# Kernel tuning notes

Measured on AMD Instinct MI355X. Metric: run time of the kernel, lower is better.

## Reference

```python
import jax, jax.numpy as jnp
import numpy as np

HEADS, DH, M, ITERS = 8, 64, 256, 6
DIM = 512


def layer_norm(x, g, b, eps=1e-5):
    mu = x.mean(-1, keepdims=True)
    var = x.var(-1, keepdims=True)
    return (x - mu) / jnp.sqrt(var + eps) * g + b


def moore_penrose_pinv(x, iters=ITERS):
    abs_x = jnp.abs(x)
    col = abs_x.sum(-1)
    row = abs_x.sum(-2)
    z = jnp.swapaxes(x, -1, -2) / (jnp.max(col) * jnp.max(row))
    I = jnp.eye(x.shape[-1], dtype=x.dtype)
    for _ in range(iters):
        xz = x @ z
        z = 0.25 * z @ (13.0 * I - xz @ (15.0 * I - xz @ (7.0 * I - xz)))
    return z


def nystrom_attn(x, w_qkv, w_out, b_out, res_w):
    b, n, _ = x.shape
    pad = (M - n % M) % M
    xp = jnp.pad(x, ((0, 0), (pad, 0), (0, 0)))  # left-pad seq as in lucidrains
    npad = n + pad
    l = npad // M  # == ceil(n / M)
    qkv = xp @ w_qkv
    q, k, v = jnp.split(qkv, 3, axis=-1)
    to_heads = lambda t: t.reshape(b, npad, HEADS, DH).transpose(0, 2, 1, 3)
    q, k, v = to_heads(q), to_heads(k), to_heads(v)
    q = q * (DH ** -0.5)
    # landmarks: mean over consecutive chunks of size l  ('(n l) d -> n d')
    ql = q.reshape(b, HEADS, M, l, DH).mean(3)
    kl = k.reshape(b, HEADS, M, l, DH).mean(3)
    a1 = jax.nn.softmax(jnp.einsum('bhid,bhjd->bhij', q, kl), -1)   # (b,h,npad,M)
    a2 = jax.nn.softmax(jnp.einsum('bhid,bhjd->bhij', ql, kl), -1)  # (b,h,M,M)
    a3 = jax.nn.softmax(jnp.einsum('bhid,bhjd->bhij', ql, k), -1)   # (b,h,M,npad)
    a2inv = moore_penrose_pinv(a2)
    out = a1 @ (a2inv @ (a3 @ v))  # (b,h,npad,DH)
    # residual depthwise conv along sequence, per head (kernel (33,1), groups=heads)
    res = jax.lax.conv_general_dilated(v, res_w, window_strides=(1, 1),
                                       padding=((16, 16), (0, 0)),
                                       dimension_numbers=('NCHW', 'OIHW', 'NCHW'),
                                       feature_group_count=HEADS)
    out = out + res
    out = out.transpose(0, 2, 1, 3).reshape(b, npad, HEADS * DH)
    out = out @ w_out + b_out
    return out[:, -n:]


def ppeg(x, w7, b7, w5, b5, w3, b3, Hh, Ww):
    B, n, C = x.shape
    cls_tok, feat = x[:, :1], x[:, 1:]
    cnn = feat.transpose(0, 2, 1).reshape(B, C, Hh, Ww)

    def dwconv(w, bb, p):
        y = jax.lax.conv_general_dilated(cnn, w, (1, 1), ((p, p), (p, p)),
                                         dimension_numbers=('NCHW', 'OIHW', 'NCHW'),
                                         feature_group_count=C)
        return y + bb[None, :, None, None]

    y = cnn + dwconv(w7, b7, 3) + dwconv(w5, b5, 2) + dwconv(w3, b3, 1)
    y = y.reshape(B, C, Hh * Ww).transpose(0, 2, 1)
    return jnp.concatenate([cls_tok, y], axis=1)


def setup_inputs() -> dict:
    key = jax.random.key(0)
    ks = iter(jax.random.split(key, 32))
    rn = lambda shape, s=0.02: jax.random.normal(next(ks), shape, dtype=jnp.float32) * s
    inp = {
        'data': jax.random.normal(next(ks), (1, 16000, 1024), dtype=jnp.float32),
        'fc1_w': rn((1024, 512)), 'fc1_b': jnp.zeros((512,), jnp.float32),
        'cls_token': rn((1, 1, 512), 1.0),
        'l1_norm_g': jnp.ones((512,), jnp.float32), 'l1_norm_b': jnp.zeros((512,), jnp.float32),
        'l1_qkv_w': rn((512, 1536)), 'l1_out_w': rn((512, 512)), 'l1_out_b': jnp.zeros((512,), jnp.float32),
        'l1_res_w': rn((8, 1, 33, 1)),
        'ppeg_w7': rn((512, 1, 7, 7)), 'ppeg_b7': jnp.zeros((512,), jnp.float32),
        'ppeg_w5': rn((512, 1, 5, 5)), 'ppeg_b5': jnp.zeros((512,), jnp.float32),
        'ppeg_w3': rn((512, 1, 3, 3)), 'ppeg_b3': jnp.zeros((512,), jnp.float32),
        'l2_norm_g': jnp.ones((512,), jnp.float32), 'l2_norm_b': jnp.zeros((512,), jnp.float32),
        'l2_qkv_w': rn((512, 1536)), 'l2_out_w': rn((512, 512)), 'l2_out_b': jnp.zeros((512,), jnp.float32),
        'l2_res_w': rn((8, 1, 33, 1)),
        'norm_g': jnp.ones((512,), jnp.float32), 'norm_b': jnp.zeros((512,), jnp.float32),
        'fc2_w': rn((512, 2)), 'fc2_b': jnp.zeros((2,), jnp.float32),
    }
    return inp


def reference(data, fc1_w, fc1_b, cls_token, l1_norm_g, l1_norm_b, l1_qkv_w, l1_out_w,
              l1_out_b, l1_res_w, ppeg_w7, ppeg_b7, ppeg_w5, ppeg_b5, ppeg_w3, ppeg_b3,
              l2_norm_g, l2_norm_b, l2_qkv_w, l2_out_w, l2_out_b, l2_res_w,
              norm_g, norm_b, fc2_w, fc2_b):
    h = jax.nn.relu(data @ fc1_w + fc1_b)  # (B, N, 512)
    N = h.shape[1]
    s = int(np.ceil(np.sqrt(N)))  # square grid side
    add = s * s - N
    h = jnp.concatenate([h, h[:, :add]], axis=1)  # repeat-pad to s*s
    B = h.shape[0]
    cls = jnp.broadcast_to(cls_token, (B, 1, h.shape[2]))
    h = jnp.concatenate([cls, h], axis=1)  # (B, s*s+1, 512)
    h = h + nystrom_attn(layer_norm(h, l1_norm_g, l1_norm_b), l1_qkv_w, l1_out_w, l1_out_b, l1_res_w)
    h = ppeg(h, ppeg_w7, ppeg_b7, ppeg_w5, ppeg_b5, ppeg_w3, ppeg_b3, s, s)
    h = h + nystrom_attn(layer_norm(h, l2_norm_g, l2_norm_b), l2_qkv_w, l2_out_w, l2_out_b, l2_res_w)
    h = layer_norm(h, norm_g, norm_b)[:, 0]
    logits = h @ fc2_w + fc2_b
    Y_prob = jax.nn.softmax(logits, -1)
    Y_hat = jnp.argmax(logits, -1)
    return logits, Y_prob, Y_hat
```

## Files before the change

### kernel.cpp

```cpp
#include <hip/hip_runtime.h>
#include <math.h>

#define NPAD   16384
#define PADR   254
#define NTOK   16130
#define NPIX   16129
#define SG     127
#define DD     512
#define NH     8
#define CHK    64

typedef __attribute__((ext_vector_type(8))) short bf16x8;
typedef __attribute__((ext_vector_type(4))) float f32x4;

__device__ __forceinline__ ushort f2bf(float f) {
  uint u = __float_as_uint(f);
  u = (u + 0x7fffu + ((u >> 16) & 1u)) >> 16;
  return (ushort)u;
}

__global__ __launch_bounds__(256) void cvt_bf_kernel(
    const float* __restrict__ src, ushort* __restrict__ dst, int n)
{
  int i = (blockIdx.x * 256 + threadIdx.x) * 8;
  if (i >= n) return;
  float4 a = *(const float4*)(src + i);
  float4 b = *(const float4*)(src + i + 4);
  bf16x8 v;
  v[0] = f2bf(a.x); v[1] = f2bf(a.y); v[2] = f2bf(a.z); v[3] = f2bf(a.w);
  v[4] = f2bf(b.x); v[5] = f2bf(b.y); v[6] = f2bf(b.z); v[7] = f2bf(b.w);
  *(bf16x8*)(dst + i) = v;
}

__global__ __launch_bounds__(256) void wtrans_bf(
    const float* __restrict__ src, ushort* __restrict__ dst, int K, int N)
{
  __shared__ float tile[32][33];
  int tx = threadIdx.x & 31, ty = threadIdx.x >> 5;
#pragma unroll
  for (int i = 0; i < 4; ++i) {
    int k = blockIdx.y * 32 + ty + i * 8, n = blockIdx.x * 32 + tx;
    tile[ty + i * 8][tx] = src[(size_t)k * N + n];
  }
  __syncthreads();
#pragma unroll
  for (int i = 0; i < 4; ++i) {
    int n = blockIdx.x * 32 + ty + i * 8, k = blockIdx.y * 32 + tx;
    dst[(size_t)n * K + k] = f2bf(tile[tx][ty + i * 8]);
  }
}

__global__ __launch_bounds__(256) void gemm_bb(
    const ushort* __restrict__ A, int lda,
    const ushort* __restrict__ Bt, int ldb,
    float* __restrict__ C, int ldc,
    int M, int K, int mode, const float* __restrict__ bias)
{
  const int t = threadIdx.x;
  const int w = t >> 6, l = t & 63, lr = l & 15, lg = l >> 4;
  const int wr = w >> 1, wc = w & 1;
  const int m0 = blockIdx.y * 128, n0 = blockIdx.x * 128;
  __shared__ __align__(16) ushort As[128 * 64];
  __shared__ __align__(16) ushort Bs[128 * 64];
  f32x4 acc[4][4];
#pragma unroll
  for (int i = 0; i < 4; ++i)
#pragma unroll
    for (int j = 0; j < 4; ++j) acc[i][j] = (f32x4){0.f, 0.f, 0.f, 0.f};

  for (int k0 = 0; k0 < K; k0 += 64) {
    __syncthreads();
#pragma unroll
    for (int i = 0; i < 4; ++i) {
      int id = t + i * 256;
      int r = id >> 3, blk = id & 7;
      int gr = m0 + r;
      bf16x8 v = (bf16x8){0, 0, 0, 0, 0, 0, 0, 0};
      if (gr < M) v = *(const bf16x8*)(A + (size_t)gr * lda + k0 + blk * 8);
      *(bf16x8*)(As + r * 64 + ((blk ^ (r & 7)) << 3)) = v;
    }
#pragma unroll
    for (int i = 0; i < 4; ++i) {
      int id = t + i * 256;
      int r = id >> 3, blk = id & 7;
      bf16x8 v = *(const bf16x8*)(Bt + (size_t)(n0 + r) * ldb + k0 + blk * 8);
      *(bf16x8*)(Bs + r * 64 + ((blk ^ (r & 7)) << 3)) = v;
    }
    __syncthreads();
    bf16x8 af[4][2], bfr[4][2];
#pragma unroll
    for (int rt = 0; rt < 4; ++rt) {
      int row = wr * 64 + rt * 16 + lr;
#pragma unroll
      for (int kc = 0; kc < 2; ++kc)
        af[rt][kc] = *(const bf16x8*)(As + row * 64 + (((kc * 4 + lg) ^ (row & 7)) << 3));
    }
#pragma unroll
    for (int nt = 0; nt < 4; ++nt) {
      int row = wc * 64 + nt * 16 + lr;
#pragma unroll
      for (int kc = 0; kc < 2; ++kc)
        bfr[nt][kc] = *(const bf16x8*)(Bs + row * 64 + (((kc * 4 + lg) ^ (row & 7)) << 3));
    }
#pragma unroll
    for (int rt = 0; rt < 4; ++rt)
#pragma unroll
      for (int nt = 0; nt < 4; ++nt) {
        acc[rt][nt] = __builtin_amdgcn_mfma_f32_16x16x32_bf16(af[rt][0], bfr[nt][0], acc[rt][nt], 0, 0, 0);
        acc[rt][nt] = __builtin_amdgcn_mfma_f32_16x16x32_bf16(af[rt][1], bfr[nt][1], acc[rt][nt], 0, 0, 0);
      }
  }
#pragma unroll
  for (int rt = 0; rt < 4; ++rt) {
#pragma unroll
// ... 24 lines not shown
  const int wr = w >> 1, wc = w & 1;
  const int m0 = blockIdx.y * 128, n0 = blockIdx.x * 128;
  __shared__ __align__(16) ushort As[128 * 64];
  __shared__ __align__(16) ushort Bs[128 * 64];
  f32x4 acc[4][4];
#pragma unroll
  for (int i = 0; i < 4; ++i)
#pragma unroll
    for (int j = 0; j < 4; ++j) acc[i][j] = (f32x4){0.f, 0.f, 0.f, 0.f};

  for (int k0 = 0; k0 < K; k0 += 64) {
    __syncthreads();
#pragma unroll
    for (int i = 0; i < 2; ++i) {
      int id = t + i * 256;
      int r = id >> 2, db = id & 3;
      const float* src = A + (size_t)(m0 + r) * lda + k0 + db * 16;
      float4 g0 = *(const float4*)(src + 0);
      float4 g1 = *(const float4*)(src + 4);
      float4 g2 = *(const float4*)(src + 8);
      float4 g3 = *(const float4*)(src + 12);
      bf16x8 e0, e1;
      e0[0] = f2bf(g0.x); e0[1] = f2bf(g0.y); e0[2] = f2bf(g0.z); e0[3] = f2bf(g0.w);
      e0[4] = f2bf(g1.x); e0[5] = f2bf(g1.y); e0[6] = f2bf(g1.z); e0[7] = f2bf(g1.w);
      e1[0] = f2bf(g2.x); e1[1] = f2bf(g2.y); e1[2] = f2bf(g2.z); e1[3] = f2bf(g2.w);
      e1[4] = f2bf(g3.x); e1[5] = f2bf(g3.y); e1[6] = f2bf(g3.z); e1[7] = f2bf(g3.w);
      ushort* dst = As + r * 64;
      *(bf16x8*)(dst + (((db * 2 + 0) ^ (r & 7)) << 3)) = e0;
      *(bf16x8*)(dst + (((db * 2 + 1) ^ (r & 7)) << 3)) = e1;
    }
#pragma unroll
    for (int i = 0; i < 4; ++i) {
      int id = t + i * 256;
      int r = id >> 3, blk = id & 7;
      bf16x8 v = *(const bf16x8*)(Bt + (size_t)(n0 + r) * ldb + k0 + blk * 8);
      *(bf16x8*)(Bs + r * 64 + ((blk ^ (r & 7)) << 3)) = v;
    }
    __syncthreads();
    bf16x8 af[4][2], bfr[4][2];
#pragma unroll
    for (int rt = 0; rt < 4; ++rt) {
      int row = wr * 64 + rt * 16 + lr;
#pragma unroll
      for (int kc = 0; kc < 2; ++kc)
        af[rt][kc] = *(const bf16x8*)(As + row * 64 + (((kc * 4 + lg) ^ (row & 7)) << 3));
    }
#pragma unroll
    for (int nt = 0; nt < 4; ++nt) {
      int row = wc * 64 + nt * 16 + lr;
#pragma unroll
      for (int kc = 0; kc < 2; ++kc)
        bfr[nt][kc] = *(const bf16x8*)(Bs + row * 64 + (((kc * 4 + lg) ^ (row & 7)) << 3));
    }
#pragma unroll
    for (int rt = 0; rt < 4; ++rt)
#pragma unroll
      for (int nt = 0; nt < 4; ++nt) {
        acc[rt][nt] = __builtin_amdgcn_mfma_f32_16x16x32_bf16(af[rt][0], bfr[nt][0], acc[rt][nt], 0, 0, 0);
        acc[rt][nt] = __builtin_amdgcn_mfma_f32_16x16x32_bf16(af[rt][1], bfr[nt][1], acc[rt][nt], 0, 0, 0);
      }
  }
#pragma unroll
  for (int rt = 0; rt < 4; ++rt) {
#pragma unroll
    for (int r = 0; r < 4; ++r) {
      int gi = m0 + wr * 64 + rt * 16 + lg * 4 + r;
      if (gi >= M) continue;
#pragma unroll
      for (int nt = 0; nt < 4; ++nt) {
        int gj = n0 + wc * 64 + nt * 16 + lr;
        float d = acc[rt][nt][r];
        if (mode == 1) d = fmaxf(d + bias[gj], 0.f);
        else if (mode == 2) { if (gj < 512) d *= 0.125f; }
        else if (mode == 3) d += C[(size_t)gi * ldc + gj] + bias[gj];
        C[(size_t)gi * ldc + gj] = d;
      }
    }
  }
}


__global__ __launch_bounds__(256) void pinv_seed(
    const float* __restrict__ a2, const float* __restrict__ red,
    float* __restrict__ z0, float* __restrict__ Y0)
{
  const int h_ = blockIdx.z;
  const int m0 = blockIdx.y * 64, n0 = blockIdx.x * 64;
  const float* Ah = a2 + (size_t)h_ * 65536;
  float* zh = z0 + (size_t)h_ * 65536;
  float* Yh = Y0 + (size_t)h_ * 65536;
  float mr = 0.f, mc = 0.f;
#pragma unroll
  for (int k = 0; k < 8; ++k) { mr = fmaxf(mr, red[k * 2]); mc = fmaxf(mc, red[k * 2 + 1]); }
  const float inv = 1.f / (mr * mc);
  const int t = threadIdx.x, w = t >> 6, l = t & 63, lr = l & 15, lg = l >> 4;
  __shared__ __align__(16) ushort Xs[64 * 64];
  __shared__ __align__(16) ushort Ys[64 * 64];
  f32x4 acc[4];
#pragma unroll
  for (int nt = 0; nt < 4; ++nt) acc[nt] = (f32x4){0.f, 0.f, 0.f, 0.f};

  for (int k0 = 0; k0 < 256; k0 += 64) {
    __syncthreads();
    {
      int r = t >> 2, db = t & 3;
      const float* src = Ah + (size_t)(m0 + r) * 256 + k0 + db * 16;
      float4 g0 = *(const float4*)(src + 0);
      float4 g1 = *(const float4*)(src + 4);
      float4 g2 = *(const float4*)(src + 8);
      float4 g3 = *(const float4*)(src + 12);
      bf16x8 e0, e1;
      e0[0] = f2bf(g0.x); e0[1] = f2bf(g0.y); e0[2] = f2bf(g0.z); e0[3] = f2bf(g0.w);
      e0[4] = f2bf(g1.x); e0[5] = f2bf(g1.y); e0[6] = f2bf(g1.z); e0[7] = f2bf(g1.w);
      e1[0] = f2bf(g2.x); e1[1] = f2bf(g2.y); e1[2] = f2bf(g2.z); e1[3] = f2bf(g2.w);
      e1[4] = f2bf(g3.x); e1[5] = f2bf(g3.y); e1[6] = f2bf(g3.z); e1[7] = f2bf(g3.w);
      ushort* dst = Xs + r * 64;
      *(bf16x8*)(dst + (((db * 2 + 0) ^ (r & 7)) << 3)) = e0;
      *(bf16x8*)(dst + (((db * 2 + 1) ^ (r & 7)) << 3)) = e1;
    }
    {
      int r = t >> 2, db = t & 3;
      const float* src = Ah + (size_t)(n0 + r) * 256 + k0 + db * 16;
      float4 g0 = *(const float4*)(src + 0);
      float4 g1 = *(const float4*)(src + 4);
      float4 g2 = *(const float4*)(src + 8);
      float4 g3 = *(const float4*)(src + 12);
      bf16x8 e0, e1;
      e0[0] = f2bf(g0.x); e0[1] = f2bf(g0.y); e0[2] = f2bf(g0.z); e0[3] = f2bf(g0.w);
      e0[4] = f2bf(g1.x); e0[5] = f2bf(g1.y); e0[6] = f2bf(g1.z); e0[7] = f2bf(g1.w);
      e1[0] = f2bf(g2.x); e1[1] = f2bf(g2.y); e1[2] = f2bf(g2.z); e1[3] = f2bf(g2.w);
      e1[4] = f2bf(g3.x); e1[5] = f2bf(g3.y); e1[6] = f2bf(g3.z); e1[7] = f2bf(g3.w);
      ushort* dst = Ys + r * 64;
      *(bf16x8*)(dst + (((db * 2 + 0) ^ (r & 7)) << 3)) = e0;
      *(bf16x8*)(dst + (((db * 2 + 1) ^ (r & 7)) << 3)) = e1;
    }
    __syncthreads();
    int arow = w * 16 + lr;
    bf16x8 af0 = *(const bf16x8*)(Xs + arow * 64 + (((0 + lg) ^ (arow & 7)) << 3));
    bf16x8 af1 = *(const bf16x8*)(Xs + arow * 64 + (((4 + lg) ^ (arow & 7)) << 3));
#pragma unroll
    for (int nt = 0; nt < 4; ++nt) {
      int brow = nt * 16 + lr;
      bf16x8 bf0 = *(const bf16x8*)(Ys + brow * 64 + (((0 + lg) ^ (brow & 7)) << 3));
      bf16x8 bf1 = *(const bf16x8*)(Ys + brow * 64 + (((4 + lg) ^ (brow & 7)) << 3));
      acc[nt] = __builtin_amdgcn_mfma_f32_16x16x32_bf16(af0, bf0, acc[nt], 0, 0, 0);
      acc[nt] = __builtin_amdgcn_mfma_f32_16x16x32_bf16(af1, bf1, acc[nt], 0, 0, 0);
    }
  }
#pragma unroll
  for (int nt = 0; nt < 4; ++nt) {
#pragma unroll
    for (int r = 0; r < 4; ++r) {
      int gi = m0 + w * 16 + lg * 4 + r;
      int gj = n0 + nt * 16 + lr;
      Yh[(size_t)gi * 256 + gj] = inv * acc[nt][r];
    }
  }
#pragma unroll
  for (int e = 0; e < 16; ++e) {
    int id = e * 256 + t;
    int i = id >> 6, j = id & 63;
    zh[(size_t)(m0 + i) * 256 + n0 + j] = inv * Ah[(size_t)(n0 + j) * 256 + m0 + i];
  }
}

__global__ __launch_bounds__(256) void nmm_A(
    const float* __restrict__ z, const float* __restrict__ Y,
    float* __restrict__ U, float* __restrict__ Y2)
{
  const int h_ = blockIdx.z & 7;
  const int job = blockIdx.z >> 3;
  const int m0 = blockIdx.y * 64, n0 = blockIdx.x * 64;
  const float* Ah = (job == 0 ? z : Y) + (size_t)h_ * 65536;
  const float* Bh = Y + (size_t)h_ * 65536;
  float* Ch = (job == 0 ? U : Y2) + (size_t)h_ * 65536;
  const int t = threadIdx.x, w = t >> 6, l = t & 63, lr = l & 15, lg = l >> 4;
  __shared__ __align__(16) ushort Xs[64 * 64];
  __shared__ __align__(16) ushort Ys[64 * 64];
  f32x4 acc[4];
#pragma unroll
  for (int nt = 0; nt < 4; ++nt) acc[nt] = (f32x4){0.f, 0.f, 0.f, 0.f};

  for (int k0 = 0; k0 < 256; k0 += 64) {
    __syncthreads();
    {
      int r = t >> 2, db = t & 3;
      const float* src = Ah + (size_t)(m0 + r) * 256 + k0 + db * 16;
      float4 g0 = *(const float4*)(src + 0);
      float4 g1 = *(const float4*)(src + 4);
      float4 g2 = *(const float4*)(src + 8);
      float4 g3 = *(const float4*)(src + 12);
      bf16x8 e0, e1;
      e0[0] = f2bf(g0.x); e0[1] = f2bf(g0.y); e0[2] = f2bf(g0.z); e0[3] = f2bf(g0.w);
      e0[4] = f2bf(g1.x); e0[5] = f2bf(g1.y); e0[6] = f2bf(g1.z); e0[7] = f2bf(g1.w);
      e1[0] = f2bf(g2.x); e1[1] = f2bf(g2.y); e1[2] = f2bf(g2.z); e1[3] = f2bf(g2.w);
      e1[4] = f2bf(g3.x); e1[5] = f2bf(g3.y); e1[6] = f2bf(g3.z); e1[7] = f2bf(g3.w);
      ushort* dst = Xs + r * 64;
      *(bf16x8*)(dst + (((db * 2 + 0) ^ (r & 7)) << 3)) = e0;
      *(bf16x8*)(dst + (((db * 2 + 1) ^ (r & 7)) << 3)) = e1;
    }
#pragma unroll
    for (int i = 0; i < 4; ++i) {
      int id = t + i * 256;
      int k = id >> 4, q = id & 15;
      float4 v = *(const float4*)(Bh + (size_t)(k0 + k) * 256 + n0 + q * 4);
      int kb = k >> 3, ke = k & 7;
      Ys[(q * 4 + 0) * 64 + ((kb ^ ((q * 4 + 0) & 7)) << 3) + ke] = f2bf(v.x);
      Ys[(q * 4 + 1) * 64 + ((kb ^ ((q * 4 + 1) & 7)) << 3) + ke] = f2bf(v.y);
      Ys[(q * 4 + 2) * 64 + ((kb ^ ((q * 4 + 2) & 7)) << 3) + ke] = f2bf(v.z);
      Ys[(q * 4 + 3) * 64 + ((kb ^ ((q * 4 + 3) & 7)) << 3) + ke] = f2bf(v.w);
    }
    __syncthreads();
    int arow = w * 16 + lr;
    bf16x8 af0 = *(const bf16x8*)(Xs + arow * 64 + (((0 + lg) ^ (arow & 7)) << 3));
    bf16x8 af1 = *(const bf16x8*)(Xs + arow * 64 + (((4 + lg) ^ (arow & 7)) << 3));
#pragma unroll
    for (int nt = 0; nt < 4; ++nt) {
      int brow = nt * 16 + lr;
      bf16x8 bf0 = *(const bf16x8*)(Ys + brow * 64 + (((0 + lg) ^ (brow & 7)) << 3));
      bf16x8 bf1 = *(const bf16x8*)(Ys + brow * 64 + (((4 + lg) ^ (brow & 7)) << 3));
      acc[nt] = __builtin_amdgcn_mfma_f32_16x16x32_bf16(af0, bf0, acc[nt], 0, 0, 0);
      acc[nt] = __builtin_amdgcn_mfma_f32_16x16x32_bf16(af1, bf1, acc[nt], 0, 0, 0);
    }
  }
#pragma unroll
  for (int nt = 0; nt < 4; ++nt) {
#pragma unroll
    for (int r = 0; r < 4; ++r) {
      int gi = m0 + w * 16 + lg * 4 + r;
      int gj = n0 + nt * 16 + lr;
      Ch[(size_t)gi * 256 + gj] = acc[nt][r];
    }
  }
}

__global__ __launch_bounds__(256) void nmm_B(
    const float* __restrict__ z, const float* __restrict__ Y,
    const float* __restrict__ U, const float* __restrict__ Y2,
    float* __restrict__ zn, float* __restrict__ yn)
{
  const int h_ = blockIdx.z & 7;
  const int job = blockIdx.z >> 3;
  const int m0 = blockIdx.y * 64, n0 = blockIdx.x * 64;
  const float* X1 = (job == 0 ? z : Y) + (size_t)h_ * 65536;
  const float* X2 = (job == 0 ? U : Y2) + (size_t)h_ * 65536;
  const float* Bh = Y2 + (size_t)h_ * 65536;
  float* Ch = (job == 0 ? zn : yn) + (size_t)h_ * 65536;
  const int t = threadIdx.x, w = t >> 6, l = t & 63, lr = l & 15, lg = l >> 4;
  __shared__ __align__(16) ushort Xs[64 * 64];
  __shared__ __align__(16) ushort Ys[64 * 64];
  f32x4 acc[4];
#pragma unroll
  for (int nt = 0; nt < 4; ++nt) acc[nt] = (f32x4){0.f, 0.f, 0.f, 0.f};

  for (int k0 = 0; k0 < 256; k0 += 64) {
    __syncthreads();
    {
      int r = t >> 2, db = t & 3;
      const float* s1 = X1 + (size_t)(m0 + r) * 256 + k0 + db * 16;
      const float* s2 = X2 + (size_t)(m0 + r) * 256 + k0 + db * 16;
      float4 a0 = *(const float4*)(s1 + 0),  b0 = *(const float4*)(s2 + 0);
      float4 a1 = *(const float4*)(s1 + 4),  b1 = *(const float4*)(s2 + 4);
      float4 a2v = *(const float4*)(s1 + 8), b2 = *(const float4*)(s2 + 8);
      float4 a3 = *(const float4*)(s1 + 12), b3 = *(const float4*)(s2 + 12);
      bf16x8 e0, e1;
      e0[0] = f2bf(7.f * a0.x - b0.x); e0[1] = f2bf(7.f * a0.y - b0.y);
      e0[2] = f2bf(7.f * a0.z - b0.z); e0[3] = f2bf(7.f * a0.w - b0.w);
      e0[4] = f2bf(7.f * a1.x - b1.x); e0[5] = f2bf(7.f * a1.y - b1.y);
      e0[6] = f2bf(7.f * a1.z - b1.z); e0[7] = f2bf(7.f * a1.w - b1.w);
      e1[0] = f2bf(7.f * a2v.x - b2.x); e1[1] = f2bf(7.f * a2v.y - b2.y);
      e1[2] = f2bf(7.f * a2v.z - b2.z); e1[3] = f2bf(7.f * a2v.w - b2.w);
      e1[4] = f2bf(7.f * a3.x - b3.x); e1[5] = f2bf(7.f * a3.y - b3.y);
      e1[6] = f2bf(7.f * a3.z - b3.z); e1[7] = f2bf(7.f * a3.w - b3.w);
      ushort* dst = Xs + r * 64;
      *(bf16x8*)(dst + (((db * 2 + 0) ^ (r & 7)) << 3)) = e0;
      *(bf16x8*)(dst + (((db * 2 + 1) ^ (r & 7)) << 3)) = e1;
    }
#pragma unroll
    for (int i = 0; i < 4; ++i) {
      int id = t + i * 256;
      int k = id >> 4, q = id & 15;
      float4 v = *(const float4*)(Bh + (size_t)(k0 + k) * 256 + n0 + q * 4);
      int kb = k >> 3, ke = k & 7;
      Ys[(q * 4 + 0) * 64 + ((kb ^ ((q * 4 + 0) & 7)) << 3) + ke] = f2bf(v.x);
      Ys[(q * 4 + 1) * 64 + ((kb ^ ((q * 4 + 1) & 7)) << 3) + ke] = f2bf(v.y);
      Ys[(q * 4 + 2) * 64 + ((kb ^ ((q * 4 + 2) & 7)) << 3) + ke] = f2bf(v.z);
      Ys[(q * 4 + 3) * 64 + ((kb ^ ((q * 4 + 3) & 7)) << 3) + ke] = f2bf(v.w);
    }
    __syncthreads();
    int arow = w * 16 + lr;
    bf16x8 af0 = *(const bf16x8*)(Xs + arow * 64 + (((0 + lg) ^ (arow & 7)) << 3));
    bf16x8 af1 = *(const bf16x8*)(Xs + arow * 64 + (((4 + lg) ^ (arow & 7)) << 3));
#pragma unroll
    for (int nt = 0; nt < 4; ++nt) {
      int brow = nt * 16 + lr;
      bf16x8 bf0 = *(const bf16x8*)(Ys + brow * 64 + (((0 + lg) ^ (brow & 7)) << 3));
      bf16x8 bf1 = *(const bf16x8*)(Ys + brow * 64 + (((4 + lg) ^ (brow & 7)) << 3));
      acc[nt] = __builtin_amdgcn_mfma_f32_16x16x32_bf16(af0, bf0, acc[nt], 0, 0, 0);
      acc[nt] = __builtin_amdgcn_mfma_f32_16x16x32_bf16(af1, bf1, acc[nt], 0, 0, 0);
    }
  }
#pragma unroll
  for (int nt = 0; nt < 4; ++nt) {
#pragma unroll
    for (int r = 0; r < 4; ++r) {
      int gi = m0 + w * 16 + lg * 4 + r;
      int gj = n0 + nt * 16 + lr;
      size_t o = (size_t)gi * 256 + gj;
      Ch[o] = 0.25f * (13.f * X1[o] - 15.f * X2[o] + acc[nt][r]);
    }
  }
}

__global__ __launch_bounds__(256) void assemble_kernel(float* __restrict__ h,
                                                       const float* __restrict__ cls)
{
  int idx = blockIdx.x * 256 + threadIdx.x;
  if (idx < 512) { h[idx] = cls[idx]; return; }
  idx -= 512;
  int i = idx >> 9, c = idx & 511;
  h[(size_t)(16001 + i) * DD + c] = h[(size_t)(1 + i) * DD + c];
}

__global__ __launch_bounds__(256) void ln_pad_kernel(
    const float* __restrict__ h, ushort* __restrict__ xn,
    const float* __restrict__ g, const float* __restrict__ b)
{
  int row = blockIdx.x;
  int t = threadIdx.x;
  if (row < PADR) {
    xn[(size_t)row * DD + t] = 0;
    xn[(size_t)row * DD + t + 256] = 0;
    return;
  }
  const float* x = h + (size_t)(row - PADR) * DD;
  __shared__ float red[256];
  float v0 = x[t], v1 = x[t + 256];
  red[t] = v0 + v1;
  __syncthreads();
  for (int s = 128; s > 0; s >>= 1) { if (t < s) red[t] += red[t + s]; __syncthreads(); }
  float mu = red[0] * (1.f / 512.f);
  __syncthreads();
  float d0 = v0 - mu, d1 = v1 - mu;
  red[t] = d0 * d0 + d1 * d1;
  __syncthreads();
  for (int s = 128; s > 0; s >>= 1) { if (t < s) red[t] += red[t + s]; __syncthreads(); }
  float rs = rsqrtf(red[0] * (1.f / 512.f) + 1e-5f);
  ushort* o = xn + (size_t)row * DD;
  o[t]       = f2bf(d0 * rs * g[t] + b[t]);
  o[t + 256] = f2bf(d1 * rs * g[t + 256] + b[t + 256]);
}

__global__ __launch_bounds__(256) void landmark_kernel(
    const float* __restrict__ qkv, float* __restrict__ ql, float* __restrict__ kl)
{
  int i = blockIdx.x;
  int c = blockIdx.y * 256 + threadIdx.x;
  const float* p = qkv + (size_t)(i * 64) * 1536 + c;
  float s = 0.f;
  for (int j = 0; j < 64; ++j) s += p[(size_t)j * 1536];
  s *= (1.f / 64.f);
  if (c < 512) ql[(size_t)i * 512 + c] = s;
  else         kl[(size_t)i * 512 + (c - 512)] = s;
}

__global__ __launch_bounds__(256) void a2_kernel(
    const float* __restrict__ ql, const float* __restrict__ kl, float* __restrict__ a2)
{
  int h_ = blockIdx.x, i = blockIdx.y;
  int t = threadIdx.x;
  __shared__ float q[64];
  __shared__ float red[256];
  if (t < 64) q[t] = ql[(size_t)i * 512 + h_ * 64 + t];
  __syncthreads();
  const float* kr = kl + (size_t)t * 512 + h_ * 64;
  float s = 0.f;
#pragma unroll
  for (int d = 0; d < 64; ++d) s = fmaf(q[d], kr[d], s);
  red[t] = s;
  __syncthreads();
  for (int st = 128; st > 0; st >>= 1) { if (t < st) red[t] = fmaxf(red[t], red[t + st]); __syncthreads(); }
  float mx = red[0];
  __syncthreads();
  float e = __expf(s - mx);
  red[t] = e;
  __syncthreads();
  for (int st = 128; st > 0; st >>= 1) { if (t < st) red[t] += red[t + st]; __syncthreads(); }
  a2[((size_t)h_ * 256 + i) * 256 + t] = e / red[0];
}

__global__ __launch_bounds__(256) void pinv_red1(const float* __restrict__ a2, float* __restrict__ red)
{
  int h_ = blockIdx.x, t = threadIdx.x;
  const float* X = a2 + (size_t)h_ * 65536;
  float rs = 0.f, cs = 0.f;
  for (int j = 0; j < 256; ++j) rs += fabsf(X[(size_t)t * 256 + j]);
  for (int i = 0; i < 256; ++i) cs += fabsf(X[(size_t)i * 256 + t]);
  __shared__ float r1[256], r2[256];
  r1[t] = rs; r2[t] = cs;
  __syncthreads();
  for (int s = 128; s > 0; s >>= 1) {
    if (t < s) { r1[t] = fmaxf(r1[t], r1[t + s]); r2[t] = fmaxf(r2[t], r2[t + s]); }
    __syncthreads();
  }
  if (t == 0) { red[h_ * 2] = r1[0]; red[h_ * 2 + 1] = r2[0]; }
}

__global__ __launch_bounds__(256) void mmb_kernel(
    const float* __restrict__ A, const float* __restrict__ B, float* __restrict__ C,
    int N, float alpha)
{
  int h_ = blockIdx.z;
  const float* Ah = A + (size_t)h_ * 256 * 256;
  const float* Bh = B + (size_t)h_ * 256 * N;
  float* Ch = C + (size_t)h_ * 256 * N;
  int m0 = blockIdx.y * 64, n0 = blockIdx.x * 64;
  __shared__ float As[16][68];
  __shared__ float Bs[16][68];
  int tid = threadIdx.x, tx = tid & 15, ty = tid >> 4;
  float acc[4][4];
#pragma unroll
  for (int i = 0; i < 4; ++i)
#pragma unroll
    for (int j = 0; j < 4; ++j) acc[i][j] = 0.f;
  for (int k0 = 0; k0 < 256; k0 += 16) {
    {
      int row = tid >> 2, k4 = (tid & 3) << 2;
      float4 v = *(const float4*)(Ah + (size_t)(m0 + row) * 256 + k0 + k4);
      As[k4 + 0][row] = v.x; As[k4 + 1][row] = v.y;
      As[k4 + 2][row] = v.z; As[k4 + 3][row] = v.w;
    }
    {
      int row = tid >> 4, c4 = (tid & 15) << 2;
      *(float4*)&Bs[row][c4] = *(const float4*)(Bh + (size_t)(k0 + row) * N + n0 + c4);
    }
    __syncthreads();
#pragma unroll
    for (int k = 0; k < 16; ++k) {
      float a[4], b[4];
      *(float4*)a = *(const float4*)&As[k][ty * 4];
      *(float4*)b = *(const float4*)&Bs[k][tx * 4];
#pragma unroll
      for (int i = 0; i < 4; ++i)
#pragma unroll
        for (int j = 0; j < 4; ++j) acc[i][j] = fmaf(a[i], b[j], acc[i][j]);
    }
    __syncthreads();
  }
#pragma unroll
  for (int i = 0; i < 4; ++i) {
    float4 r;
    r.x = alpha * acc[i][0]; r.y = alpha * acc[i][1];
    r.z = alpha * acc[i][2]; r.w = alpha * acc[i][3];
    *(float4*)(Ch + (size_t)(m0 + ty * 4 + i) * N + n0 + tx * 4) = r;
  }
}

__global__ __launch_bounds__(256) void a3v_mfma(
    const float* __restrict__ qkv, const float* __restrict__ ql,
    float* __restrict__ pacc, float* __restrict__ den)
{
  const int h_ = blockIdx.x;
  const int ch = blockIdx.y;
  const int t  = threadIdx.x;
  const int w  = t >> 6;
  const int l  = t & 63;
  const int lr = l & 15;
  const int lg = l >> 4;

  __shared__ __align__(16) ushort kls[64 * 64];
  __shared__ __align__(16) ushort vls[80 * 64];
  __shared__ __align__(16) ushort pls[4][64 * 64];

  bf16x8 qf[4][2];
#pragma unroll
  for (int rt = 0; rt < 4; ++rt)
#pragma unroll
    for (int dc = 0; dc < 2; ++dc) {
      const float* p = ql + (size_t)(64 * w + rt * 16 + lr) * 512 + h_ * 64 + dc * 32 + lg * 8;
      float4 f0 = *(const float4*)p;
      float4 f1 = *(const float4*)(p + 4);
      bf16x8 v;
      v[0] = f2bf(f0.x); v[1] = f2bf(f0.y); v[2] = f2bf(f0.z); v[3] = f2bf(f0.w);
      v[4] = f2bf(f1.x); v[5] = f2bf(f1.y); v[6] = f2bf(f1.z); v[7] = f2bf(f1.w);
      qf[rt][dc] = v;
    }

  if (t < 128) {
    int rr = t >> 3, cb = t & 7;
    ushort val = (rr == 0) ? (ushort)0x3f80 : (ushort)0;
    bf16x8 vv;
#pragma unroll
    for (int k = 0; k < 8; ++k) vv[k] = (short)val;
    *(bf16x8*)(vls + (64 + rr) * 64 + ((cb ^ (rr & 7)) << 3)) = vv;
  }

  f32x4 acc[4][5];
#pragma unroll
  for (int rt = 0; rt < 4; ++rt)
#pragma unroll
    for (int dt = 0; dt < 5; ++dt) acc[rt][dt] = (f32x4){0.f, 0.f, 0.f, 0.f};

  const int j0base = ch * 256;
  for (int jt = 0; jt < 4; ++jt) {
    const int j0 = j0base + jt * 64;
    __syncthreads();
    {
      int r = t >> 2, db = t & 3;
      const float* src = qkv + (size_t)(j0 + r) * 1536 + 512 + h_ * 64 + db * 16;
      float4 g0 = *(const float4*)(src + 0);
      float4 g1 = *(const float4*)(src + 4);
      float4 g2 = *(const float4*)(src + 8);
      float4 g3 = *(const float4*)(src + 12);
// ... 358 lines not shown
  __syncthreads();
  for (int s = 128; s > 0; s >>= 1) { if (t < s) red[t] += red[t + s]; __syncthreads(); }
  float rs = rsqrtf(red[0] * (1.f / 512.f) + 1e-5f);
  __syncthreads();
  float x0 = d0 * rs * g[t] + b[t];
  float x1 = d1 * rs * g[t + 256] + b[t + 256];
  red[t] = x0 * w[t * 2] + x1 * w[(t + 256) * 2];
  __syncthreads();
  for (int s = 128; s > 0; s >>= 1) { if (t < s) red[t] += red[t + s]; __syncthreads(); }
  float l0 = red[0] + bias[0];
  __syncthreads();
  red[t] = x0 * w[t * 2 + 1] + x1 * w[(t + 256) * 2 + 1];
  __syncthreads();
  for (int s = 128; s > 0; s >>= 1) { if (t < s) red[t] += red[t + s]; __syncthreads(); }
  float l1 = red[0] + bias[1];
  if (t == 0) {
    out[0] = l0; out[1] = l1;
    float mx = fmaxf(l0, l1);
    float e0 = __expf(l0 - mx), e1 = __expf(l1 - mx);
    float inv = 1.f / (e0 + e1);
    out[2] = e0 * inv; out[3] = e1 * inv;
    out[4] = (l1 > l0) ? 1.f : 0.f;
  }
}

extern "C" void kernel_launch(void* const* d_in, const int* in_sizes, int n_in,
                              void* d_out, int out_size, void* d_ws, size_t ws_size,
                              hipStream_t stream)
{
  const float* data   = (const float*)d_in[0];
  const float* fc1_w  = (const float*)d_in[1];
  const float* fc1_b  = (const float*)d_in[2];
  const float* cls    = (const float*)d_in[3];
  const float* l1_g   = (const float*)d_in[4];
  const float* l1_b   = (const float*)d_in[5];
  const float* l1_qkv = (const float*)d_in[6];
  const float* l1_ow  = (const float*)d_in[7];
  const float* l1_ob  = (const float*)d_in[8];
  const float* l1_rw  = (const float*)d_in[9];
  const float* w7     = (const float*)d_in[10];
  const float* b7     = (const float*)d_in[11];
  const float* w5     = (const float*)d_in[12];
  const float* b5     = (const float*)d_in[13];
  const float* w3     = (const float*)d_in[14];
  const float* b3     = (const float*)d_in[15];
  const float* l2_g   = (const float*)d_in[16];
  const float* l2_b   = (const float*)d_in[17];
  const float* l2_qkv = (const float*)d_in[18];
  const float* l2_ow  = (const float*)d_in[19];
  const float* l2_ob  = (const float*)d_in[20];
  const float* l2_rw  = (const float*)d_in[21];
  const float* ng     = (const float*)d_in[22];
  const float* nb     = (const float*)d_in[23];
  const float* fc2_w  = (const float*)d_in[24];
  const float* fc2_b  = (const float*)d_in[25];
  float* out = (float*)d_out;

  float* ws   = (float*)d_ws;
  float* h    = ws;
  float* xn   = h    + (size_t)16384 * 512;
  float* qkv  = xn   + (size_t)16384 * 512;
  float* attn = qkv  + (size_t)16384 * 1536;
  float* ql   = attn + (size_t)16384 * 512;
  float* kl   = ql   + 256 * 512;
  float* a2b  = kl   + 256 * 512;
  float* z0   = a2b  + 8 * 256 * 256;
  float* z1   = z0   + 8 * 256 * 256;
  float* xzb  = z1   + 8 * 256 * 256;
  float* tb   = xzb  + 8 * 256 * 256;
  float* ub   = tb   + 8 * 256 * 256;
  float* a3v  = ub   + 8 * 256 * 256;
  float* w2   = a3v  + 8 * 256 * 64;
  float* pacc = w2   + 8 * 256 * 64;
  float* pms  = pacc + (size_t)8 * 32 * 256 * 64;
  float* red  = pms  + (size_t)8 * 32 * 256 * 2;
  float* wtb  = red  + 32;

  ushort* fc1_wt  = (ushort*)pacc;
  ushort* qkv_wt0 = fc1_wt + 512 * 1024;
  ushort* qkv_wt1 = qkv_wt0 + 1536 * 512;
  ushort* out_wt0 = qkv_wt1 + 1536 * 512;
  ushort* out_wt1 = out_wt0 + 512 * 512;

  float* yb0 = pacc + 1310720;
  float* yb1 = yb0 + 8 * 256 * 256;

  ushort* xnb    = (ushort*)xn;
  ushort* databf = (ushort*)qkv;

  float* a3v_pacc = xn;
  float* a3v_den  = pms;

  wtrans_bf<<<dim3(16, 32), 256, 0, stream>>>(fc1_w, fc1_wt, 1024, 512);
  wtrans_bf<<<dim3(48, 16), 256, 0, stream>>>(l1_qkv, qkv_wt0, 512, 1536);
  wtrans_bf<<<dim3(48, 16), 256, 0, stream>>>(l2_qkv, qkv_wt1, 512, 1536);
  wtrans_bf<<<dim3(16, 16), 256, 0, stream>>>(l1_ow, out_wt0, 512, 512);
  wtrans_bf<<<dim3(16, 16), 256, 0, stream>>>(l2_ow, out_wt1, 512, 512);
  wtrans_kernel<<<2, 256, 0, stream>>>(w7, w5, w3, wtb);
  cvt_bf_kernel<<<8000, 256, 0, stream>>>(data, databf, 16000 * 1024);

  gemm_bb<<<dim3(4, 125), 256, 0, stream>>>(databf, 1024, fc1_wt, 1024, h + 512, 512,
                                            16000, 1024, 1, fc1_b);
  assemble_kernel<<<260, 256, 0, stream>>>(h, cls);

  for (int layer = 0; layer < 2; ++layer) {
    const float* gg = layer ? l2_g   : l1_g;
    const float* bb = layer ? l2_b   : l1_b;
    const ushort* qw = layer ? qkv_wt1 : qkv_wt0;
    const ushort* ow = layer ? out_wt1 : out_wt0;
    const float* ob = layer ? l2_ob  : l1_ob;
    const float* rw = layer ? l2_rw  : l1_rw;

    ln_pad_kernel<<<16384, 256, 0, stream>>>(h, xnb, gg, bb);
    gemm_bb<<<dim3(12, 128), 256, 0, stream>>>(xnb, 512, qw, 512, qkv, 1536,
                                               16384, 512, 2, nullptr);
    landmark_kernel<<<dim3(256, 4), 256, 0, stream>>>(qkv, ql, kl);
    a2_kernel<<<dim3(8, 256), 256, 0, stream>>>(ql, kl, a2b);
    pinv_red1<<<8, 256, 0, stream>>>(a2b, red);
    pinv_seed<<<dim3(4, 4, 8), 256, 0, stream>>>(a2b, red, z0, yb0);
    float* zc = z0; float* zn = z1; float* yc = yb0; float* yn = yb1;
    for (int it = 0; it < 6; ++it) {
      nmm_A<<<dim3(4, 4, 16), 256, 0, stream>>>(zc, yc, ub, tb);
      nmm_B<<<dim3(4, 4, 16), 256, 0, stream>>>(zc, yc, ub, tb, zn, yn);
      float* s = zc; zc = zn; zn = s;
      s = yc; yc = yn; yn = s;
    }
    a3v_mfma<<<dim3(8, CHK), 256, 0, stream>>>(qkv, ql, a3v_pacc, a3v_den);
    a3v_merge_kernel<<<dim3(8, 256), 64, 0, stream>>>(a3v_pacc, a3v_den, a3v);
    mmb_kernel<<<dim3(1, 4, 8), 256, 0, stream>>>(zc, a3v, w2, 64, 1.f);
    a1_mfma<<<dim3(8, 64), 256, 0, stream>>>(qkv, kl, w2, attn);
    resconv_kernel<<<dim3(2048, 2), 256, 0, stream>>>(qkv, rw, attn);
    gemm_bt<<<dim3(4, 127), 256, 0, stream>>>(attn + (size_t)254 * 512, 512, ow, 512,
                                              h, 512, 16130, 512, 3, ob);
    if (layer == 0) {
      ppeg_kernel<<<dim3(127 * 4, 8), 256, 0, stream>>>(h, qkv, wtb, b7, b5, b3);
      hipMemcpyAsync(h + 512, qkv, (size_t)16129 * 512 * 4,
                     hipMemcpyDeviceToDevice, stream);
    }
  }
  final_kernel<<<1, 256, 0, stream>>>(h, ng, nb, fc2_w, fc2_b, out);
}
```

Baseline: 946.7 us.

## Store Newton-Schulz pinv iterates in bf16 and drop separate input conversion

Stores the pseudo-inverse iterates (z, Y, U, Y2) in bf16 rather than fp32, so the small nmm kernels load bf16x8 vectors directly and skip per-element conversion. It also removes the standalone fp32-to-bf16 conversion pass over the input and calls gemm_bt on the fp32 data for fc1. Less memory traffic and one fewer kernel launch, at the cost of extra rounding error accumulating across the six iterations. The fc1 GEMM now goes through a different, possibly less efficient kernel path.

```diff
diff --git a/kernel.cpp b/kernel.cpp
--- a/kernel.cpp
+++ b/kernel.cpp
@@ -18,18 +18,8 @@
   u = (u + 0x7fffu + ((u >> 16) & 1u)) >> 16;
   return (ushort)u;
 }
-
-__global__ __launch_bounds__(256) void cvt_bf_kernel(
-    const float* __restrict__ src, ushort* __restrict__ dst, int n)
-{
-  int i = (blockIdx.x * 256 + threadIdx.x) * 8;
-  if (i >= n) return;
-  float4 a = *(const float4*)(src + i);
-  float4 b = *(const float4*)(src + i + 4);
-  bf16x8 v;
-  v[0] = f2bf(a.x); v[1] = f2bf(a.y); v[2] = f2bf(a.z); v[3] = f2bf(a.w);
-  v[4] = f2bf(b.x); v[5] = f2bf(b.y); v[6] = f2bf(b.z); v[7] = f2bf(b.w);
-  *(bf16x8*)(dst + i) = v;
+__device__ __forceinline__ float bf2f(ushort u) {
+  return __uint_as_float((uint)u << 16);
 }
 
 __global__ __launch_bounds__(256) void wtrans_bf(
@@ -220,13 +210,13 @@
 
 __global__ __launch_bounds__(256) void pinv_seed(
     const float* __restrict__ a2, const float* __restrict__ red,
-    float* __restrict__ z0, float* __restrict__ Y0)
+    ushort* __restrict__ z0, ushort* __restrict__ Y0)
 {
   const int h_ = blockIdx.z;
   const int m0 = blockIdx.y * 64, n0 = blockIdx.x * 64;
   const float* Ah = a2 + (size_t)h_ * 65536;
-  float* zh = z0 + (size_t)h_ * 65536;
-  float* Yh = Y0 + (size_t)h_ * 65536;
+  ushort* zh = z0 + (size_t)h_ * 65536;
+  ushort* Yh = Y0 + (size_t)h_ * 65536;
   float mr = 0.f, mc = 0.f;
 #pragma unroll
   for (int k = 0; k < 8; ++k) { mr = fmaxf(mr, red[k * 2]); mc = fmaxf(mc, red[k * 2 + 1]); }
@@ -291,27 +281,27 @@
     for (int r = 0; r < 4; ++r) {
       int gi = m0 + w * 16 + lg * 4 + r;
       int gj = n0 + nt * 16 + lr;
-      Yh[(size_t)gi * 256 + gj] = inv * acc[nt][r];
+      Yh[(size_t)gi * 256 + gj] = f2bf(inv * acc[nt][r]);
     }
   }
 #pragma unroll
   for (int e = 0; e < 16; ++e) {
     int id = e * 256 + t;
     int i = id >> 6, j = id & 63;
-    zh[(size_t)(m0 + i) * 256 + n0 + j] = inv * Ah[(size_t)(n0 + j) * 256 + m0 + i];
+    zh[(size_t)(m0 + i) * 256 + n0 + j] = f2bf(inv * Ah[(size_t)(n0 + j) * 256 + m0 + i]);
   }
 }
 
 __global__ __launch_bounds__(256) void nmm_A(
-    const float* __restrict__ z, const float* __restrict__ Y,
-    float* __restrict__ U, float* __restrict__ Y2)
+    const ushort* __restrict__ z, const ushort* __restrict__ Y,
+    ushort* __restrict__ U, ushort* __restrict__ Y2)
 {
   const int h_ = blockIdx.z & 7;
   const int job = blockIdx.z >> 3;
   const int m0 = blockIdx.y * 64, n0 = blockIdx.x * 64;
-  const float* Ah = (job == 0 ? z : Y) + (size_t)h_ * 65536;
-  const float* Bh = Y + (size_t)h_ * 65536;
-  float* Ch = (job == 0 ? U : Y2) + (size_t)h_ * 65536;
+  const ushort* Ah = (job == 0 ? z : Y) + (size_t)h_ * 65536;
+  const ushort* Bh = Y + (size_t)h_ * 65536;
+  ushort* Ch = (job == 0 ? U : Y2) + (size_t)h_ * 65536;
   const int t = threadIdx.x, w = t >> 6, l = t & 63, lr = l & 15, lg = l >> 4;
   __shared__ __align__(16) ushort Xs[64 * 64];
   __shared__ __align__(16) ushort Ys[64 * 64];
@@ -321,32 +311,23 @@
 
   for (int k0 = 0; k0 < 256; k0 += 64) {
     __syncthreads();
-    {
-      int r = t >> 2, db = t & 3;
-      const float* src = Ah + (size_t)(m0 + r) * 256 + k0 + db * 16;
-      float4 g0 = *(const float4*)(src + 0);
-      float4 g1 = *(const float4*)(src + 4);
-      float4 g2 = *(const float4*)(src + 8);
-      float4 g3 = *(const float4*)(src + 12);
-      bf16x8 e0, e1;
-      e0[0] = f2bf(g0.x); e0[1] = f2bf(g0.y); e0[2] = f2bf(g0.z); e0[3] = f2bf(g0.w);
-      e0[4] = f2bf(g1.x); e0[5] = f2bf(g1.y); e0[6] = f2bf(g1.z); e0[7] = f2bf(g1.w);
-      e1[0] = f2bf(g2.x); e1[1] = f2bf(g2.y); e1[2] = f2bf(g2.z); e1[3] = f2bf(g2.w);
-      e1[4] = f2bf(g3.x); e1[5] = f2bf(g3.y); e1[6] = f2bf(g3.z); e1[7] = f2bf(g3.w);
-      ushort* dst = Xs + r * 64;
-      *(bf16x8*)(dst + (((db * 2 + 0) ^ (r & 7)) << 3)) = e0;
-      *(bf16x8*)(dst + (((db * 2 + 1) ^ (r & 7)) << 3)) = e1;
+#pragma unroll
+    for (int i = 0; i < 2; ++i) {
+      int id = t + i * 256;
+      int r = id >> 3, blk = id & 7;
+      bf16x8 v = *(const bf16x8*)(Ah + (size_t)(m0 + r) * 256 + k0 + blk * 8);
+      *(bf16x8*)(Xs + r * 64 + ((blk ^ (r & 7)) << 3)) = v;
     }
 #pragma unroll
     for (int i = 0; i < 4; ++i) {
       int id = t + i * 256;
       int k = id >> 4, q = id & 15;
-      float4 v = *(const float4*)(Bh + (size_t)(k0 + k) * 256 + n0 + q * 4);
+      ushort4 v = *(const ushort4*)(Bh + (size_t)(k0 + k) * 256 + n0 + q * 4);
       int kb = k >> 3, ke = k & 7;
-      Ys[(q * 4 + 0) * 64 + ((kb ^ ((q * 4 + 0) & 7)) << 3) + ke] = f2bf(v.x);
-      Ys[(q * 4 + 1) * 64 + ((kb ^ ((q * 4 + 1) & 7)) << 3) + ke] = f2bf(v.y);
-      Ys[(q * 4 + 2) * 64 + ((kb ^ ((q * 4 + 2) & 7)) << 3) + ke] = f2bf(v.z);
-      Ys[(q * 4 + 3) * 64 + ((kb ^ ((q * 4 + 3) & 7)) << 3) + ke] = f2bf(v.w);
+      Ys[(q * 4 + 0) * 64 + ((kb ^ ((q * 4 + 0) & 7)) << 3) + ke] = v.x;
+      Ys[(q * 4 + 1) * 64 + ((kb ^ ((q * 4 + 1) & 7)) << 3) + ke] = v.y;
+      Ys[(q * 4 + 2) * 64 + ((kb ^ ((q * 4 + 2) & 7)) << 3) + ke] = v.z;
+      Ys[(q * 4 + 3) * 64 + ((kb ^ ((q * 4 + 3) & 7)) << 3) + ke] = v.w;
     }
     __syncthreads();
     int arow = w * 16 + lr;
@@ -367,23 +348,23 @@
     for (int r = 0; r < 4; ++r) {
       int gi = m0 + w * 16 + lg * 4 + r;
       int gj = n0 + nt * 16 + lr;
-      Ch[(size_t)gi * 256 + gj] = acc[nt][r];
+      Ch[(size_t)gi * 256 + gj] = f2bf(acc[nt][r]);
     }
   }
 }
 
 __global__ __launch_bounds__(256) void nmm_B(
-    const float* __restrict__ z, const float* __restrict__ Y,
-    const float* __restrict__ U, const float* __restrict__ Y2,
-    float* __restrict__ zn, float* __restrict__ yn)
+    const ushort* __restrict__ z, const ushort* __restrict__ Y,
+    const ushort* __restrict__ U, const ushort* __restrict__ Y2,
+    ushort* __restrict__ zn, ushort* __restrict__ yn)
 {
   const int h_ = blockIdx.z & 7;
   const int job = blockIdx.z >> 3;
   const int m0 = blockIdx.y * 64, n0 = blockIdx.x * 64;
-  const float* X1 = (job == 0 ? z : Y) + (size_t)h_ * 65536;
-  const float* X2 = (job == 0 ? U : Y2) + (size_t)h_ * 65536;
-  const float* Bh = Y2 + (size_t)h_ * 65536;
-  float* Ch = (job == 0 ? zn : yn) + (size_t)h_ * 65536;
+  const ushort* X1 = (job == 0 ? z : Y) + (size_t)h_ * 65536;
+  const ushort* X2 = (job == 0 ? U : Y2) + (size_t)h_ * 65536;
+  const ushort* Bh = Y2 + (size_t)h_ * 65536;
+  ushort* Ch = (job == 0 ? zn : yn) + (size_t)h_ * 65536;
   const int t = threadIdx.x, w = t >> 6, l = t & 63, lr = l & 15, lg = l >> 4;
   __shared__ __align__(16) ushort Xs[64 * 64];
   __shared__ __align__(16) ushort Ys[64 * 64];
@@ -393,37 +374,28 @@
 
   for (int k0 = 0; k0 < 256; k0 += 64) {
     __syncthreads();
-    {
-      int r = t >> 2, db = t & 3;
-      const float* s1 = X1 + (size_t)(m0 + r) * 256 + k0 + db * 16;
-      const float* s2 = X2 + (size_t)(m0 + r) * 256 + k0 + db * 16;
-      float4 a0 = *(const float4*)(s1 + 0),  b0 = *(const float4*)(s2 + 0);
-      float4 a1 = *(const float4*)(s1 + 4),  b1 = *(const float4*)(s2 + 4);
-      float4 a2v = *(const float4*)(s1 + 8), b2 = *(const float4*)(s2 + 8);
-      float4 a3 = *(const float4*)(s1 + 12), b3 = *(const float4*)(s2 + 12);
-      bf16x8 e0, e1;
-      e0[0] = f2bf(7.f * a0.x - b0.x); e0[1] = f2bf(7.f * a0.y - b0.y);
-      e0[2] = f2bf(7.f * a0.z - b0.z); e0[3] = f2bf(7.f * a0.w - b0.w);
-      e0[4] = f2bf(7.f * a1.x - b1.x); e0[5] = f2bf(7.f * a1.y - b1.y);
-      e0[6] = f2bf(7.f * a1.z - b1.z); e0[7] = f2bf(7.f * a1.w - b1.w);
-      e1[0] = f2bf(7.f * a2v.x - b2.x); e1[1] = f2bf(7.f * a2v.y - b2.y);
-      e1[2] = f2bf(7.f * a2v.z - b2.z); e1[3] = f2bf(7.f * a2v.w - b2.w);
-      e1[4] = f2bf(7.f * a3.x - b3.x); e1[5] = f2bf(7.f * a3.y - b3.y);
-      e1[6] = f2bf(7.f * a3.z - b3.z); e1[7] = f2bf(7.f * a3.w - b3.w);
-      ushort* dst = Xs + r * 64;
-      *(bf16x8*)(dst + (((db * 2 + 0) ^ (r & 7)) << 3)) = e0;
-      *(bf16x8*)(dst + (((db * 2 + 1) ^ (r & 7)) << 3)) = e1;
+#pragma unroll
+    for (int i = 0; i < 2; ++i) {
+      int id = t + i * 256;
+      int r = id >> 3, blk = id & 7;
+      bf16x8 a = *(const bf16x8*)(X1 + (size_t)(m0 + r) * 256 + k0 + blk * 8);
+      bf16x8 b = *(const bf16x8*)(X2 + (size_t)(m0 + r) * 256 + k0 + blk * 8);
+      bf16x8 e;
+#pragma unroll
+      for (int j = 0; j < 8; ++j)
+        e[j] = f2bf(7.f * bf2f((ushort)a[j]) - bf2f((ushort)b[j]));
+      *(bf16x8*)(Xs + r * 64 + ((blk ^ (r & 7)) << 3)) = e;
     }
 #pragma unroll
     for (int i = 0; i < 4; ++i) {
       int id = t + i * 256;
       int k = id >> 4, q = id & 15;
-      float4 v = *(const float4*)(Bh + (size_t)(k0 + k) * 256 + n0 + q * 4);
+      ushort4 v = *(const ushort4*)(Bh + (size_t)(k0 + k) * 256 + n0 + q * 4);
       int kb = k >> 3, ke = k & 7;
-      Ys[(q * 4 + 0) * 64 + ((kb ^ ((q * 4 + 0) & 7)) << 3) + ke] = f2bf(v.x);
-      Ys[(q * 4 + 1) * 64 + ((kb ^ ((q * 4 + 1) & 7)) << 3) + ke] = f2bf(v.y);
-      Ys[(q * 4 + 2) * 64 + ((kb ^ ((q * 4 + 2) & 7)) << 3) + ke] = f2bf(v.z);
-      Ys[(q * 4 + 3) * 64 + ((kb ^ ((q * 4 + 3) & 7)) << 3) + ke] = f2bf(v.w);
+      Ys[(q * 4 + 0) * 64 + ((kb ^ ((q * 4 + 0) & 7)) << 3) + ke] = v.x;
+      Ys[(q * 4 + 1) * 64 + ((kb ^ ((q * 4 + 1) & 7)) << 3) + ke] = v.y;
+      Ys[(q * 4 + 2) * 64 + ((kb ^ ((q * 4 + 2) & 7)) << 3) + ke] = v.z;
+      Ys[(q * 4 + 3) * 64 + ((kb ^ ((q * 4 + 3) & 7)) << 3) + ke] = v.w;
     }
     __syncthreads();
     int arow = w * 16 + lr;
@@ -445,7 +417,7 @@
       int gi = m0 + w * 16 + lg * 4 + r;
       int gj = n0 + nt * 16 + lr;
       size_t o = (size_t)gi * 256 + gj;
-      Ch[o] = 0.25f * (13.f * X1[o] - 15.f * X2[o] + acc[nt][r]);
+      Ch[o] = f2bf(0.25f * (13.f * bf2f(X1[o]) - 15.f * bf2f(X2[o]) + acc[nt][r]));
     }
   }
 }
@@ -545,11 +517,11 @@
 }
 
 __global__ __launch_bounds__(256) void mmb_kernel(
-    const float* __restrict__ A, const float* __restrict__ B, float* __restrict__ C,
+    const ushort* __restrict__ A, const float* __restrict__ B, float* __restrict__ C,
     int N, float alpha)
 {
   int h_ = blockIdx.z;
-  const float* Ah = A + (size_t)h_ * 256 * 256;
+  const ushort* Ah = A + (size_t)h_ * 256 * 256;
   const float* Bh = B + (size_t)h_ * 256 * N;
   float* Ch = C + (size_t)h_ * 256 * N;
   int m0 = blockIdx.y * 64, n0 = blockIdx.x * 64;
@@ -564,9 +536,9 @@
   for (int k0 = 0; k0 < 256; k0 += 16) {
     {
       int row = tid >> 2, k4 = (tid & 3) << 2;
-      float4 v = *(const float4*)(Ah + (size_t)(m0 + row) * 256 + k0 + k4);
-      As[k4 + 0][row] = v.x; As[k4 + 1][row] = v.y;
-      As[k4 + 2][row] = v.z; As[k4 + 3][row] = v.w;
+      ushort4 v = *(const ushort4*)(Ah + (size_t)(m0 + row) * 256 + k0 + k4);
+      As[k4 + 0][row] = bf2f(v.x); As[k4 + 1][row] = bf2f(v.y);
+      As[k4 + 2][row] = bf2f(v.z); As[k4 + 3][row] = bf2f(v.w);
     }
     {
       int row = tid >> 4, c4 = (tid & 15) << 2;
@@ -1091,11 +1063,14 @@
   ushort* out_wt0 = qkv_wt1 + 1536 * 512;
   ushort* out_wt1 = out_wt0 + 512 * 512;
 
-  float* yb0 = pacc + 1310720;
-  float* yb1 = yb0 + 8 * 256 * 256;
-
-  ushort* xnb    = (ushort*)xn;
-  ushort* databf = (ushort*)qkv;
+  ushort* zb0 = (ushort*)z0;
+  ushort* zb1 = (ushort*)z1;
+  ushort* Ub  = (ushort*)ub;
+  ushort* Y2b = (ushort*)tb;
+  ushort* yb0 = (ushort*)(pacc + 1310720);
+  ushort* yb1 = yb0 + 8 * 256 * 256;
+
+  ushort* xnb = (ushort*)xn;
 
   float* a3v_pacc = xn;
   float* a3v_den  = pms;
@@ -1106,9 +1081,8 @@
   wtrans_bf<<<dim3(16, 16), 256, 0, stream>>>(l1_ow, out_wt0, 512, 512);
   wtrans_bf<<<dim3(16, 16), 256, 0, stream>>>(l2_ow, out_wt1, 512, 512);
   wtrans_kernel<<<2, 256, 0, stream>>>(w7, w5, w3, wtb);
-  cvt_bf_kernel<<<8000, 256, 0, stream>>>(data, databf, 16000 * 1024);
-
-  gemm_bb<<<dim3(4, 125), 256, 0, stream>>>(databf, 1024, fc1_wt, 1024, h + 512, 512,
+
+  gemm_bt<<<dim3(4, 125), 256, 0, stream>>>(data, 1024, fc1_wt, 1024, h + 512, 512,
                                             16000, 1024, 1, fc1_b);
   assemble_kernel<<<260, 256, 0, stream>>>(h, cls);
 
@@ -1126,12 +1100,12 @@
     landmark_kernel<<<dim3(256, 4), 256, 0, stream>>>(qkv, ql, kl);
     a2_kernel<<<dim3(8, 256), 256, 0, stream>>>(ql, kl, a2b);
     pinv_red1<<<8, 256, 0, stream>>>(a2b, red);
-    pinv_seed<<<dim3(4, 4, 8), 256, 0, stream>>>(a2b, red, z0, yb0);
-    float* zc = z0; float* zn = z1; float* yc = yb0; float* yn = yb1;
+    pinv_seed<<<dim3(4, 4, 8), 256, 0, stream>>>(a2b, red, zb0, yb0);
+    ushort* zc = zb0; ushort* zn = zb1; ushort* yc = yb0; ushort* yn = yb1;
     for (int it = 0; it < 6; ++it) {
-      nmm_A<<<dim3(4, 4, 16), 256, 0, stream>>>(zc, yc, ub, tb);
-      nmm_B<<<dim3(4, 4, 16), 256, 0, stream>>>(zc, yc, ub, tb, zn, yn);
-      float* s = zc; zc = zn; zn = s;
+      nmm_A<<<dim3(4, 4, 16), 256, 0, stream>>>(zc, yc, Ub, Y2b);
+      nmm_B<<<dim3(4, 4, 16), 256, 0, stream>>>(zc, yc, Ub, Y2b, zn, yn);
+      ushort* s = zc; zc = zn; zn = s;
       s = yc; yc = yn; yn = s;
     }
     a3v_mfma<<<dim3(8, CHK), 256, 0, stream>>>(qkv, ql, a3v_pacc, a3v_den);
```

After: 967.0 us. 1.02x slower.
